# Kernel tuning notes

Hardware: AMD Instinct MI355X
Metric: run time of the kernel (lower is better)

The kernel has to match this reference:

```python
import jax, jax.numpy as jnp
import numpy as np

B, L, C = 8, 2048, 512
R, H, DK = 256, 8, 64
MASK_NEG = -2.0**15 + 1.0


def setup_inputs() -> dict:
    key = jax.random.key(0)
    ks = jax.random.split(key, 9)
    s = 1.0 / np.sqrt(C)
    return {
        "qx": jax.random.normal(ks[0], (B, L, C), jnp.float32),
        "kx": jax.random.normal(ks[1], (B, L, C), jnp.float32),
        "vx": jax.random.normal(ks[2], (B, L, C), jnp.float32),
        "addLoss": jnp.zeros((), jnp.float32),
        "maskPAD": jnp.ones((B, L, L), jnp.bool_),
        "Wp": jax.random.normal(ks[3], (R, C), jnp.float32) * s,
        "WQ": jax.random.normal(ks[4], (H * DK, C), jnp.float32) * s,
        "WK": jax.random.normal(ks[5], (H * DK, C), jnp.float32) * s,
        "WV": jax.random.normal(ks[6], (H * DK, C), jnp.float32) * s,
        "WO": jax.random.normal(ks[7], (C, H * DK), jnp.float32) * (1.0 / np.sqrt(H * DK)),
    }


def reference(qx, kx, vx, addLoss, maskPAD, Wp, WQ, WK, WV, WO):
    # linearLevel == 'l1', dropout treated as identity (eval), training losses included
    b, l, c = qx.shape
    r = Wp.shape[0]
    offI = (1.0 - jnp.eye(r, dtype=qx.dtype))  # ones_minus_I, [r, r]

    pScore = jnp.einsum('blc,rc->blr', vx, Wp)                       # [B, L, r]
    pad = (maskPAD[:, 0] == 0)                                       # [B, L]
    pScore = jnp.where(pad[:, :, None], MASK_NEG, pScore)
    pAlpha = jnp.swapaxes(jax.nn.softmax(pScore, axis=-2), -1, -2)   # [B, r, L]
    pAlpha_ = jax.nn.softmax(pScore, axis=-1)                        # [B, L, r]

    addLoss = addLoss + jnp.mean((jnp.einsum('brl,bsl->brs', pAlpha, pAlpha) * offI) ** 2)

    qr = pAlpha @ qx                                                 # [B, r, C]
    kr = pAlpha @ kx
    vr = pAlpha @ vx

    queries = (qr @ WQ.T).reshape(b, r, H, DK).transpose(0, 2, 1, 3)  # [B, H, r, dk]
    keys = (kr @ WK.T).reshape(b, r, H, DK).transpose(0, 2, 1, 3)
    values = (vr @ WV.T).reshape(b, r, H, DK).transpose(0, 2, 1, 3)

    scores = jnp.einsum('bhrd,bhsd->bhrs', queries, keys) / jnp.asarray(np.sqrt(DK), qx.dtype)
    alpha = jax.nn.softmax(scores, axis=-1)                          # [B, H, r, r]
    addLoss = addLoss + jnp.mean(alpha * offI)

    z = alpha @ values                                               # [B, H, r, dk]
    z = z.transpose(0, 2, 1, 3).reshape(b, r, H * DK)
    z = z @ WO.T                                                     # [B, r, C]

    addLoss = addLoss + jnp.mean((jnp.einsum('blr,bls->brs', pAlpha_, pAlpha_) * offI) ** 2)
    z = pAlpha_ @ z                                                  # [B, L, C]
    return z, scores, addLoss
```

## Files before the change

kernel.cpp:

```cpp
#include <hip/hip_runtime.h>

#define B_  8
#define L_  2048
#define C_  512
#define R_  256
#define H_  8
#define DK_ 64
#define HD_ 512
#define MASK_NEG (-32767.0f)

typedef __attribute__((ext_vector_type(8))) short short8;
typedef __attribute__((ext_vector_type(8))) unsigned short ushort8;
typedef __attribute__((ext_vector_type(4))) unsigned short ushort4_t;
typedef __attribute__((ext_vector_type(4))) float f32x4;
typedef unsigned short u16;

__device__ inline u16 bf16_rne(float x) {
    unsigned u = __float_as_uint(x);
    return (u16)((u + 0x7FFFu + ((u >> 16) & 1u)) >> 16);
}
__device__ inline unsigned cvt_hl(float x) {
    u16 hh = bf16_rne(x);
    float hf = __uint_as_float(((unsigned)hh) << 16);
    u16 ll = bf16_rne(x - hf);
    return (unsigned)hh | ((unsigned)ll << 16);
}

struct Ptr3 { const void* p0; const void* p1; const void* p2; };

__device__ inline float waveMax(float v) {
    #pragma unroll
    for (int o = 32; o; o >>= 1) v = fmaxf(v, __shfl_xor(v, o, 64));
    return v;
}
__device__ inline float waveSum(float v) {
    #pragma unroll
    for (int o = 32; o; o >>= 1) v += __shfl_xor(v, o, 64);
    return v;
}

#define GLL16(g, l) __builtin_amdgcn_global_load_lds( \
    (const __attribute__((address_space(1))) void*)(g), \
    (__attribute__((address_space(3))) void*)(l), 16, 0, 0)

template<int BN, int AMODE, int BMODE, int EPI, bool TRIPLE, int NTERM = 3, int KSPLIT = 1>
__global__ __launch_bounds__(256) void gemm_pl(
    Ptr3 aH, Ptr3 aL, Ptr3 bH, Ptr3 bL, Ptr3 cH, Ptr3 cL,
    Ptr3 cT1, Ptr3 cT2, int ldct, long long csT,
    int K, int lda, int ldb, int ldc, int divz,
    long long ash, long long bsh, long long csh,
    long long asb, long long bsb, long long csb,
    long long ksa, long long ksb, long long ksc,
    float scale)
{
    constexpr int NF = BN / 32;
    constexpr int XA = (NTERM == 3) ? 64 : 1;
    constexpr int XB = (NTERM == 3) ? BN : 1;
    __shared__ u16 Ahs[64][40], Als[XA][40];
    __shared__ u16 Bhs[BN][40], Bls[XB][40];

    const int gx = gridDim.x, gy = gridDim.y;
    const int nwg = gx * gy * gridDim.z;
    int flat = blockIdx.x + gx * (blockIdx.y + gy * blockIdx.z);
    {
        int q = nwg >> 3;
        int xcd = flat & 7, idx = flat >> 3;
        flat = xcd * q + idx;
    }
    const int bx = flat % gx;
    const int by = (flat / gx) % gy;
    const int z  = flat / (gx * gy);

    const int zb = z / divz;
    const int rem = z - zb * divz;
    const int zh = rem / KSPLIT, ks = rem - zh * KSPLIT;
    const int Keff = K / KSPLIT;
    const void* avH = TRIPLE ? (zb == 0 ? aH.p0 : zb == 1 ? aH.p1 : aH.p2) : aH.p0;
    const void* avL = TRIPLE ? (zb == 0 ? aL.p0 : zb == 1 ? aL.p1 : aL.p2) : aL.p0;
    const void* bvH = TRIPLE ? (zb == 0 ? bH.p0 : zb == 1 ? bH.p1 : bH.p2) : bH.p0;
    const void* bvL = TRIPLE ? (zb == 0 ? bL.p0 : zb == 1 ? bL.p1 : bL.p2) : bL.p0;
    void* cvH = (void*)(TRIPLE ? (zb == 0 ? cH.p0 : zb == 1 ? cH.p1 : cH.p2) : cH.p0);
    void* cvL = (void*)(TRIPLE ? (zb == 0 ? cL.p0 : zb == 1 ? cL.p1 : cL.p2) : cL.p0);
    void* cvT1 = (void*)(TRIPLE ? (zb == 0 ? cT1.p0 : zb == 1 ? cT1.p1 : cT1.p2) : cT1.p0);
    void* cvT2 = (void*)(TRIPLE ? (zb == 0 ? cT2.p0 : zb == 1 ? cT2.p1 : cT2.p2) : cT2.p0);
    const long long ao = (TRIPLE ? 0 : (long long)zb * asb) + (long long)zh * ash + (long long)ks * ksa;
    const long long bo = (TRIPLE ? 0 : (long long)zb * bsb) + (long long)zh * bsh + (long long)ks * ksb;
    const long long co = (TRIPLE ? 0 : (long long)zb * csb) + (long long)zh * csh + (long long)ks * ksc;
    const long long coT = (long long)zh * csT;

    const u16*   AHg = (const u16*)avH + ao;
    const u16*   ALg = (const u16*)avL + ao;
    const u16*   BHg = (const u16*)bvH + bo;
    const u16*   BLg = (const u16*)bvL + bo;
    const float* Bfg = (const float*)bvH + bo;
    float* Cf  = (float*)cvH + co;
    u16*   CHg = (u16*)cvH + co;
    u16*   CLg = (u16*)cvL + co;

    const int m0 = by * 64, n0 = bx * BN;
    const int tid = threadIdx.x;
    const int lane = tid & 63, w = tid >> 6;
    const int wrow = (w >> 1) * 32, wcol = (w & 1) * (BN / 2);
    const int l15 = lane & 15, lg = lane >> 4;

    f32x4 zero = {0.f, 0.f, 0.f, 0.f};
    f32x4 acc[2][NF];
    #pragma unroll
    for (int mf = 0; mf < 2; ++mf)
        #pragma unroll
        for (int nf = 0; nf < NF; ++nf) acc[mf][nf] = zero;

    for (int k0 = 0; k0 < Keff; k0 += 32) {
        {
            int row = tid >> 2, kc = (tid & 3) << 3;
            long long off = (long long)(m0 + row) * lda + (k0 + kc);
            *(ushort8*)&Ahs[row][kc] = *(const ushort8*)(AHg + off);
            if constexpr (NTERM == 3)
                *(ushort8*)&Als[row][kc] = *(const ushort8*)(ALg + off);
        }
        if (BMODE == 0) {
            #pragma unroll
            for (int t = tid; t < BN * 4; t += 256) {
                int row = t >> 2, kc = (t & 3) << 3;
                long long off = (long long)(n0 + row) * ldb + (k0 + kc);
                *(ushort8*)&Bhs[row][kc] = *(const ushort8*)(BHg + off);
                if constexpr (NTERM == 3)
                    *(ushort8*)&Bls[row][kc] = *(const ushort8*)(BLg + off);
            }
        } else {
            #pragma unroll
            for (int t = tid; t < BN * 4; t += 256) {
                int row = t >> 2, kc = (t & 3) << 3;
                const float* s = Bfg + (long long)(n0 + row) * ldb + (k0 + kc);
                float4 v0 = *(const float4*)s, v1 = *(const float4*)(s + 4);
                unsigned p0 = cvt_hl(v0.x), p1 = cvt_hl(v0.y), p2 = cvt_hl(v0.z), p3 = cvt_hl(v0.w);
                unsigned p4 = cvt_hl(v1.x), p5 = cvt_hl(v1.y), p6 = cvt_hl(v1.z), p7 = cvt_hl(v1.w);
                ushort8 h, l;
                h[0]=(u16)p0; h[1]=(u16)p1; h[2]=(u16)p2; h[3]=(u16)p3;
                h[4]=(u16)p4; h[5]=(u16)p5; h[6]=(u16)p6; h[7]=(u16)p7;
                l[0]=(u16)(p0>>16); l[1]=(u16)(p1>>16); l[2]=(u16)(p2>>16); l[3]=(u16)(p3>>16);
                l[4]=(u16)(p4>>16); l[5]=(u16)(p5>>16); l[6]=(u16)(p6>>16); l[7]=(u16)(p7>>16);
                *(ushort8*)&Bhs[row][kc] = h;
                if constexpr (NTERM == 3)
                    *(ushort8*)&Bls[row][kc] = l;
            }
        }
        __syncthreads();

        short8 a_h[2], a_l[2];
        a_h[0] = *(const short8*)&Ahs[wrow +      l15][lg * 8];
        a_h[1] = *(const short8*)&Ahs[wrow + 16 + l15][lg * 8];
        if constexpr (NTERM == 3) {
            a_l[0] = *(const short8*)&Als[wrow +      l15][lg * 8];
            a_l[1] = *(const short8*)&Als[wrow + 16 + l15][lg * 8];
        }
        #pragma unroll
        for (int nf = 0; nf < NF; ++nf) {
            short8 b_h = *(const short8*)&Bhs[wcol + nf * 16 + l15][lg * 8];
            if constexpr (NTERM == 3) {
                short8 b_l = *(const short8*)&Bls[wcol + nf * 16 + l15][lg * 8];
                #pragma unroll
                for (int mf = 0; mf < 2; ++mf) {
                    acc[mf][nf] = __builtin_amdgcn_mfma_f32_16x16x32_bf16(a_h[mf], b_h, acc[mf][nf], 0, 0, 0);
                    acc[mf][nf] = __builtin_amdgcn_mfma_f32_16x16x32_bf16(a_h[mf], b_l, acc[mf][nf], 0, 0, 0);
                    acc[mf][nf] = __builtin_amdgcn_mfma_f32_16x16x32_bf16(a_l[mf], b_h, acc[mf][nf], 0, 0, 0);
                }
            } else {
                #pragma unroll
                for (int mf = 0; mf < 2; ++mf)
                    acc[mf][nf] = __builtin_amdgcn_mfma_f32_16x16x32_bf16(a_h[mf], b_h, acc[mf][nf], 0, 0, 0);
            }
        }
        __syncthreads();
    }

    #pragma unroll
    for (int mf = 0; mf < 2; ++mf)
        #pragma unroll
        for (int nf = 0; nf < NF; ++nf) {
            int row = m0 + wrow + mf * 16 + lg * 4;
            int col = n0 + wcol + nf * 16 + l15;
            if constexpr (EPI == 0 || EPI == 3) {
                #pragma unroll
                for (int j = 0; j < 4; ++j)
                    Cf[(long long)(row + j) * ldc + col] = acc[mf][nf][j] * scale;
                if constexpr (EPI == 3) {
                    float* CfT = (float*)cvT1 + coT;
                    float4 v = make_float4(acc[mf][nf][0] * scale, acc[mf][nf][1] * scale,
                                           acc[mf][nf][2] * scale, acc[mf][nf][3] * scale);
                    *(float4*)(CfT + (long long)col * ldct + row) = v;
                }
            } else {
                unsigned p[4];
                #pragma unroll
                for (int j = 0; j < 4; ++j) {
                    p[j] = cvt_hl(acc[mf][nf][j] * scale);
                    if constexpr (EPI != 5) {
                        CHg[(long long)(row + j) * ldc + col] = (u16)p[j];
                        CLg[(long long)(row + j) * ldc + col] = (u16)(p[j] >> 16);
                    }
                }
                if constexpr (EPI == 4 || EPI == 5) {
                    u16* CTH = (u16*)cvT1 + coT;
                    u16* CTL = (u16*)cvT2 + coT;
                    ushort4_t h, l;
                    #pragma unroll
                    for (int j = 0; j < 4; ++j) { h[j] = (u16)p[j]; l[j] = (u16)(p[j] >> 16); }
                    *(ushort4_t*)(CTH + (long long)col * ldct + row) = h;
                    *(ushort4_t*)(CTL + (long long)col * ldct + row) = l;
                }
            }
        }
}

template<int EPI, bool TRIPLE, int NTERM, int KSPLIT, bool TRIANG = false>
__global__ __launch_bounds__(256) void gemm_gll(
    Ptr3 aH, Ptr3 aL, Ptr3 bH, Ptr3 bL, Ptr3 cH, Ptr3 cL,
    Ptr3 cT1, Ptr3 cT2, int ldct, long long csT,
    int K, int lda, int ldb, int ldc, int divz,
    long long ash, long long bsh, long long csh,
    long long ksa, long long ksb, long long ksc,
    float scale,
    const float* addLossIn = nullptr, const float* lossAcc = nullptr,
    const float* offArr = nullptr, float* lossOut = nullptr)
{
    constexpr int XA = (NTERM == 3) ? 128 : 1;
    __shared__ u16 Ahs[2][128][32];
    __shared__ u16 Bhs[2][128][32];
    __shared__ u16 Als[XA][32], Bls[XA][32];
    __shared__ float red2[4];

    const int gx = gridDim.x, gy = gridDim.y;
    const int nwg = gx * gy * gridDim.z;
    int flat = blockIdx.x + gx * (blockIdx.y + gy * blockIdx.z);
    {
        int q = nwg >> 3;
        int xcd = flat & 7, idx = flat >> 3;
        flat = xcd * q + idx;
    }
    const int bx = flat % gx;
    const int by = (flat / gx) % gy;
    const int z  = flat / (gx * gy);

    const int zb = z / divz;
    const int rem = z - zb * divz;
    const int zh = rem / KSPLIT, ks = rem - zh * KSPLIT;
    const int Keff = K / KSPLIT;
    const void* avH = TRIPLE ? (zb == 0 ? aH.p0 : zb == 1 ? aH.p1 : aH.p2) : aH.p0;
    const void* avL = TRIPLE ? (zb == 0 ? aL.p0 : zb == 1 ? aL.p1 : aL.p2) : aL.p0;
    const void* bvH = TRIPLE ? (zb == 0 ? bH.p0 : zb == 1 ? bH.p1 : bH.p2) : bH.p0;
    const void* bvL = TRIPLE ? (zb == 0 ? bL.p0 : zb == 1 ? bL.p1 : bL.p2) : bL.p0;
    void* cvH = (void*)(TRIPLE ? (zb == 0 ? cH.p0 : zb == 1 ? cH.p1 : cH.p2) : cH.p0);
    void* cvL = (void*)(TRIPLE ? (zb == 0 ? cL.p0 : zb == 1 ? cL.p1 : cL.p2) : cL.p0);
    void* cvT1 = (void*)(TRIPLE ? (zb == 0 ? cT1.p0 : zb == 1 ? cT1.p1 : cT1.p2) : cT1.p0);
    void* cvT2 = (void*)(TRIPLE ? (zb == 0 ? cT2.p0 : zb == 1 ? cT2.p1 : cT2.p2) : cT2.p0);
    const long long ao = (long long)zh * ash + (long long)ks * ksa;
    const long long bo = (long long)zh * bsh + (long long)ks * ksb;
    const long long co = (long long)zh * csh + (long long)ks * ksc;
    const long long coT = (long long)zh * csT;

    const u16* AHg = (const u16*)avH + ao;
    const u16* ALg = (const u16*)avL + ao;
    const u16* BHg = (const u16*)bvH + bo;
    const u16* BLg = (const u16*)bvL + bo;
    float* Cf  = (float*)cvH + co;
    u16*   CHg = (u16*)cvH + co;
    u16*   CLg = (u16*)cvL + co;

    int m0, n0;
    if constexpr (TRIANG) {
        m0 = (bx >= 1) ? 128 : 0;
        n0 = (bx == 2) ? 128 : 0;
    } else {
        m0 = by * 128; n0 = bx * 128;
    }
    const int tid = threadIdx.x;
    const int lane = tid & 63, w = tid >> 6;
    const int wrow = (w >> 1) * 64, wcol = (w & 1) * 64;
    const int l15 = lane & 15, lg = lane >> 4;

    f32x4 zero = {0.f, 0.f, 0.f, 0.f};
    f32x4 acc[4][4];
    #pragma unroll
    for (int mf = 0; mf < 4; ++mf)
        #pragma unroll
        for (int nf = 0; nf < 4; ++nf) acc[mf][nf] = zero;

    const int ric = lane >> 2;
    const int cc  = lane & 3;

    auto STAGE_HI = [&](int bufsel, int k0) {
        #pragma unroll
        for (int i = 0; i < 2; ++i) {
            int chunk = w * 2 + i;
            int row = chunk * 16 + ric;
            int gcol = ((cc ^ ((row >> 1) & 3)) << 3);
            GLL16(AHg + (long long)(m0 + row) * lda + (k0 + gcol), &Ahs[bufsel][chunk * 16][0]);
            GLL16(BHg + (long long)(n0 + row) * ldb + (k0 + gcol), &Bhs[bufsel][chunk * 16][0]);
        }
    };
    auto STAGE_LO = [&](int k0) {
        #pragma unroll
        for (int i = 0; i < 2; ++i) {
            int chunk = w * 2 + i;
            int row = chunk * 16 + ric;
            int gcol = ((cc ^ ((row >> 1) & 3)) << 3);
            GLL16(ALg + (long long)(m0 + row) * lda + (k0 + gcol), &Als[chunk * 16][0]);
            GLL16(BLg + (long long)(n0 + row) * ldb + (k0 + gcol), &Bls[chunk * 16][0]);
        }
    };

    const int nt = Keff / 32;
    int cur = 0;
    STAGE_HI(0, 0);

    for (int t = 0; t < nt; ++t) {
        if constexpr (NTERM == 3) STAGE_LO(t * 32);
        if (t + 1 < nt) {
            STAGE_HI(cur ^ 1, (t + 1) * 32);
            asm volatile("s_waitcnt vmcnt(4)" ::: "memory");
        } else {
            asm volatile("s_waitcnt vmcnt(0)" ::: "memory");
        }
        __builtin_amdgcn_s_barrier();

        short8 a_h[4], a_l[4];
        #pragma unroll
        for (int mf = 0; mf < 4; ++mf) {
            int ar = wrow + mf * 16 + l15;
            int ac = (lg ^ ((ar >> 1) & 3)) << 3;
            a_h[mf] = *(const short8*)&Ahs[cur][ar][ac];
            if constexpr (NTERM == 3) a_l[mf] = *(const short8*)&Als[ar][ac];
        }
        __builtin_amdgcn_s_setprio(1);
        #pragma unroll
        for (int nf = 0; nf < 4; ++nf) {
            int br = wcol + nf * 16 + l15;
            int bc = (lg ^ ((br >> 1) & 3)) << 3;
            short8 b_h = *(const short8*)&Bhs[cur][br][bc];
            if constexpr (NTERM == 3) {
                short8 b_l = *(const short8*)&Bls[br][bc];
                #pragma unroll
                for (int mf = 0; mf < 4; ++mf) {
                    acc[mf][nf] = __builtin_amdgcn_mfma_f32_16x16x32_bf16(a_h[mf], b_h, acc[mf][nf], 0, 0, 0);
                    acc[mf][nf] = __builtin_amdgcn_mfma_f32_16x16x32_bf16(a_h[mf], b_l, acc[mf][nf], 0, 0, 0);
                    acc[mf][nf] = __builtin_amdgcn_mfma_f32_16x16x32_bf16(a_l[mf], b_h, acc[mf][nf], 0, 0, 0);
                }
            } else {
                #pragma unroll
                for (int mf = 0; mf < 4; ++mf)
                    acc[mf][nf] = __builtin_amdgcn_mfma_f32_16x16x32_bf16(a_h[mf], b_h, acc[mf][nf], 0, 0, 0);
            }
        }
        __builtin_amdgcn_s_setprio(0);
        __builtin_amdgcn_s_barrier();
        cur ^= 1;
    }

    #pragma unroll
    for (int mf = 0; mf < 4; ++mf)
        #pragma unroll
        for (int nf = 0; nf < 4; ++nf) {
            int row = m0 + wrow + mf * 16 + lg * 4;
            int col = n0 + wcol + nf * 16 + l15;
            if constexpr (EPI == 0) {
                #pragma unroll
                for (int j = 0; j < 4; ++j)
                    Cf[(long long)(row + j) * ldc + col] = acc[mf][nf][j] * scale;
            } else {
                unsigned p[4];
                #pragma unroll
                for (int j = 0; j < 4; ++j) p[j] = cvt_hl(acc[mf][nf][j] * scale);
                if (cvH) {
                    #pragma unroll
                    for (int j = 0; j < 4; ++j) {
                        CHg[(long long)(row + j) * ldc + col] = (u16)p[j];
                        CLg[(long long)(row + j) * ldc + col] = (u16)(p[j] >> 16);
                    }
                }
                if constexpr (EPI == 3) {
                    if (cvT1) {
                        u16* CTH = (u16*)cvT1 + coT;
                        u16* CTL = (u16*)cvT2 + coT;
                        ushort4_t h, l;
                        #pragma unroll
                        for (int j = 0; j < 4; ++j) { h[j] = (u16)p[j]; l[j] = (u16)(p[j] >> 16); }
                        *(ushort4_t*)(CTH + (long long)col * ldct + row) = h;
                        *(ushort4_t*)(CTL + (long long)col * ldct + row) = l;
                    }
                }
            }
        }

    if (lossOut != nullptr && flat == 0) {
        float s = 0.0f;
        for (int i = tid; i < B_ * H_ * R_; i += 256) s += offArr[i];
        s = waveSum(s);
        if (lane == 0) red2[w] = s;
        __syncthreads();
        if (tid == 0) {
            float total = red2[0] + red2[1] + red2[2] + red2[3];
            lossOut[0] = addLossIn[0]
                       + lossAcc[0] * (1.0f / ((float)B_ * R_ * R_))
                       + total      * (1.0f / ((float)B_ * H_ * R_ * R_))
                       + lossAcc[2] * (1.0f / ((float)B_ * R_ * R_));
        }
    }
}

#define KS_ 4
#define NKS6_ 2
__global__ __launch_bounds__(256) void reduce_all(
    const float* __restrict__ G1, const float* __restrict__ G2,
    int nks, float* __restrict__ lossBase,
    const float* __restrict__ Cpart, Ptr3 dstH, Ptr3 dstL)
{
    __shared__ float red[4];
    int lane = threadIdx.x & 63, wid = threadIdx.x >> 6;
    if (blockIdx.x < 1024) {
        const long long N = (long long)B_ * R_ * R_;
        int seg = blockIdx.x >> 9;
        const float* G = seg ? G2 : G1;
        float* lossDst = lossBase + (seg ? 2 : 0);
        long long i4 = ((long long)(blockIdx.x & 511) * 256 + threadIdx.x) << 2;
        float s = 0.0f;
        if (i4 < N) {
            int e = (int)(i4 & (long long)(R_ * R_ - 1));
            int row = e >> 8, c0 = e & 255;
            if (!(row < 128 && c0 >= 128)) {
                float4 g = make_float4(0.f, 0.f, 0.f, 0.f);
                for (int ks = 0; ks < nks; ++ks) {
                    float4 v = *(const float4*)(G + (long long)ks * N + i4);
                    g.x += v.x; g.y += v.y; g.z += v.z; g.w += v.w;
                }
                float wgt = (row >= 128 && c0 < 128) ? 2.0f : 1.0f;
                if (row != c0 + 0) s += wgt * g.x * g.x;
                if (row != c0 + 1) s += wgt * g.y * g.y;
                if (row != c0 + 2) s += wgt * g.z * g.z;
                if (row != c0 + 3) s += wgt * g.w * g.w;
            }
        }
        #pragma unroll
        for (int o = 32; o; o >>= 1) s += __shfl_down(s, o, 64);
        if (lane == 0) red[wid] = s;
        __syncthreads();
        if (threadIdx.x == 0) atomicAdd(lossDst, red[0] + red[1] + red[2] + red[3]);
    } else {
        const long long T = (long long)B_ * R_ * C_;
        long long i4 = (long long)(blockIdx.x - 1024) * 256 + threadIdx.x;
        if (i4 >= 3 * (T >> 2)) return;
        int member = (int)(i4 / (T >> 2));
        long long rem = (i4 - (long long)member * (T >> 2)) << 2;
        float4 a = *(const float4*)(Cpart + (long long)member * T + rem);
        #pragma unroll
        for (int ks = 1; ks < NKS6_; ++ks) {
            float4 b = *(const float4*)(Cpart + (long long)ks * 3 * T + (long long)member * T + rem);
            a.x += b.x; a.y += b.y; a.z += b.z; a.w += b.w;
        }
        unsigned q0 = cvt_hl(a.x), q1 = cvt_hl(a.y), q2 = cvt_hl(a.z), q3 = cvt_hl(a.w);
        ushort4_t h, l;
        h[0]=(u16)q0; h[1]=(u16)q1; h[2]=(u16)q2; h[3]=(u16)q3;
        l[0]=(u16)(q0>>16); l[1]=(u16)(q1>>16); l[2]=(u16)(q2>>16); l[3]=(u16)(q3>>16);
        u16* dH = (u16*)(member == 0 ? dstH.p0 : member == 1 ? dstH.p1 : dstH.p2);
        u16* dL = (u16*)(member == 0 ? dstL.p0 : member == 1 ? dstL.p1 : dstL.p2);
        *(ushort4_t*)(dH + rem) = h;
        *(ushort4_t*)(dL + rem) = l;
    }
}

__global__ __launch_bounds__(256) void xpose_f32p3(
    Ptr3 src, Ptr3 dstH, Ptr3 dstL,
    int M, int N, long long ibs, long long obs, int divz)
{
    __shared__ float S[64][65];
    int z = blockIdx.z;
    int m = z / divz, b = z - m * divz;
    const float* ip = (const float*)(m == 0 ? src.p0 : m == 1 ? src.p1 : src.p2)
                      + (long long)b * ibs;
    u16* opH = (u16*)(m == 0 ? dstH.p0 : m == 1 ? dstH.p1 : dstH.p2) + (long long)b * obs;
    u16* opL = (u16*)(m == 0 ? dstL.p0 : m == 1 ? dstL.p1 : dstL.p2) + (long long)b * obs;
    int n0 = blockIdx.x * 64, m0 = blockIdx.y * 64;
    int t = threadIdx.x;
    int c4 = (t & 15) << 2, rq = t >> 4;
    #pragma unroll
    for (int p = 0; p < 4; ++p) {
        int r = p * 16 + rq;
        float4 v = *(const float4*)(ip + (long long)(m0 + r) * N + n0 + c4);
        S[r][c4+0]=v.x; S[r][c4+1]=v.y; S[r][c4+2]=v.z; S[r][c4+3]=v.w;
    }
    __syncthreads();
    #pragma unroll
    for (int p = 0; p < 4; ++p) {
        int nr = p * 16 + rq;
        unsigned q0 = cvt_hl(S[c4+0][nr]), q1 = cvt_hl(S[c4+1][nr]);
        unsigned q2 = cvt_hl(S[c4+2][nr]), q3 = cvt_hl(S[c4+3][nr]);
        ushort4_t h, l;
        h[0]=(u16)q0; h[1]=(u16)q1; h[2]=(u16)q2; h[3]=(u16)q3;
        l[0]=(u16)(q0>>16); l[1]=(u16)(q1>>16); l[2]=(u16)(q2>>16); l[3]=(u16)(q3>>16);
        long long ob = (long long)(n0 + nr) * M + m0 + c4;
        *(ushort4_t*)(opH + ob) = h;
        *(ushort4_t*)(opL + ob) = l;
    }
}

__global__ __launch_bounds__(256) void xpose_u16p(
    const u16* __restrict__ inH, const u16* __restrict__ inL,
    u16* __restrict__ outH, u16* __restrict__ outL,
    int M, int N, long long ibs, long long obs)
{
    __shared__ u16 SH[64][66], SL[64][66];
    const u16* ipH = inH + (long long)blockIdx.z * ibs;
    const u16* ipL = inL + (long long)blockIdx.z * ibs;
    u16* opH = outH + (long long)blockIdx.z * obs;
    u16* opL = outL + (long long)blockIdx.z * obs;
    int n0 = blockIdx.x * 64, m0 = blockIdx.y * 64;
    int t = threadIdx.x;
    int c4 = (t & 15) << 2, rq = t >> 4;
    #pragma unroll
    for (int p = 0; p < 4; ++p) {
        int r = p * 16 + rq;
        long long ib = (long long)(m0 + r) * N + n0 + c4;
        ushort4_t vh = *(const ushort4_t*)(ipH + ib);
        ushort4_t vl = *(const ushort4_t*)(ipL + ib);
        SH[r][c4+0]=vh[0]; SH[r][c4+1]=vh[1]; SH[r][c4+2]=vh[2]; SH[r][c4+3]=vh[3];
        SL[r][c4+0]=vl[0]; SL[r][c4+1]=vl[1]; SL[r][c4+2]=vl[2]; SL[r][c4+3]=vl[3];
    }
    __syncthreads();
    #pragma unroll
    for (int p = 0; p < 4; ++p) {
        int nr = p * 16 + rq;
        ushort4_t h, l;
        h[0]=SH[c4+0][nr]; h[1]=SH[c4+1][nr]; h[2]=SH[c4+2][nr]; h[3]=SH[c4+3][nr];
        l[0]=SL[c4+0][nr]; l[1]=SL[c4+1][nr]; l[2]=SL[c4+2][nr]; l[3]=SL[c4+3][nr];
        long long ob = (long long)(n0 + nr) * M + m0 + c4;
        *(ushort4_t*)(opH + ob) = h;
        *(ushort4_t*)(opL + ob) = l;
    }
}

__global__ __launch_bounds__(256) void conv_planes5(
    const float* __restrict__ s0, const float* __restrict__ s1, const float* __restrict__ s2,
    const float* __restrict__ s3, const float* __restrict__ s4,
    u16* h0, u16* l0, u16* h1, u16* l1, u16* h2, u16* l2,
    u16* h3, u16* l3, u16* h4, u16* l4,
    float* __restrict__ lossZero)
{
    if (blockIdx.x == 0 && threadIdx.x < 3) lossZero[threadIdx.x] = 0.0f;
    const int N0 = 32768, NW = 65536;
    int i = blockIdx.x * 256 + threadIdx.x;
    if (i >= N0 + 4 * NW) return;
    const float* s; u16* h; u16* l; int off;
    if (i < N0) { s = s0; h = h0; l = l0; off = i; }
    else {
        int j = i - N0, seg = j / NW;
        off = j - seg * NW;
        s = seg == 0 ? s1 : seg == 1 ? s2 : seg == 2 ? s3 : s4;
        h = seg == 0 ? h1 : seg == 1 ? h2 : seg == 2 ? h3 : h4;
        l = seg == 0 ? l1 : seg == 1 ? l2 : seg == 2 ? l3 : l4;
    }
    float4 v = ((const float4*)s)[off];
    unsigned p0 = cvt_hl(v.x), p1 = cvt_hl(v.y), p2 = cvt_hl(v.z), p3 = cvt_hl(v.w);
    ushort4_t hv, lv;
    hv[0]=(u16)p0; hv[1]=(u16)p1; hv[2]=(u16)p2; hv[3]=(u16)p3;
    lv[0]=(u16)(p0>>16); lv[1]=(u16)(p1>>16); lv[2]=(u16)(p2>>16); lv[3]=(u16)(p3>>16);
    ((ushort4_t*)h)[off] = hv;
    ((ushort4_t*)l)[off] = lv;
}

__global__ __launch_bounds__(256) void softmax_both(
    const float* __restrict__ pT, const float* __restrict__ pScore,
    const int* __restrict__ mask,
    u16* __restrict__ ltH, u16* __restrict__ ltL,
    u16* __restrict__ rH, u16* __restrict__ rL)
{
    __shared__ float sm[4], ss[4];
    int bxid = blockIdx.x;
    int lane = threadIdx.x & 63, wid = threadIdx.x >> 6;
    if (bxid < B_ * R_) {
        int zi = bxid;
        int b = zi >> 8;
        const float* row = pT + (long long)zi * L_;
        const int* mk = mask + (long long)b * L_ * L_;
        float vals[8];
        float mx = -3.4e38f;
        #pragma unroll
        for (int i = 0; i < 8; ++i) {
            int l = threadIdx.x + i * 256;
            float v = row[l];
            if (mk[l] == 0) v = MASK_NEG;
            vals[i] = v; mx = fmaxf(mx, v);
        }
        mx = waveMax(mx);
        if (lane == 0) sm[wid] = mx;
        __syncthreads();
        mx = fmaxf(fmaxf(sm[0], sm[1]), fmaxf(sm[2], sm[3]));
        float sum = 0.0f;
        #pragma unroll
        for (int i = 0; i < 8; ++i) { float e = __expf(vals[i] - mx); vals[i] = e; sum += e; }
        sum = waveSum(sum);
        if (lane == 0) ss[wid] = sum;
        __syncthreads();
        sum = ss[0] + ss[1] + ss[2] + ss[3];
        float inv = 1.0f / sum;
        long long base = (long long)zi * L_;
        #pragma unroll
        for (int i = 0; i < 8; ++i) {
            unsigned p = cvt_hl(vals[i] * inv);
            ltH[base + threadIdx.x + i * 256] = (u16)p;
            ltL[base + threadIdx.x + i * 256] = (u16)(p >> 16);
        }
    } else {
        long long z = (long long)(bxid - B_ * R_) * 4 + wid;
        int b = (int)(z >> 11), l = (int)(z & 2047);
        bool pad = (mask[(long long)b * L_ * L_ + l] == 0);
        float4 v = *(const float4*)(pScore + z * R_ + lane * 4);
        if (pad) { v.x = MASK_NEG; v.y = MASK_NEG; v.z = MASK_NEG; v.w = MASK_NEG; }
        float mx = waveMax(fmaxf(fmaxf(v.x, v.y), fmaxf(v.z, v.w)));
        float e0 = __expf(v.x - mx), e1 = __expf(v.y - mx);
        float e2 = __expf(v.z - mx), e3 = __expf(v.w - mx);
        float inv = 1.0f / waveSum(e0 + e1 + e2 + e3);
        unsigned p0 = cvt_hl(e0 * inv), p1 = cvt_hl(e1 * inv);
        unsigned p2 = cvt_hl(e2 * inv), p3 = cvt_hl(e3 * inv);
        ushort4_t h, lo;
        h[0]=(u16)p0; h[1]=(u16)p1; h[2]=(u16)p2; h[3]=(u16)p3;
        lo[0]=(u16)(p0>>16); lo[1]=(u16)(p1>>16); lo[2]=(u16)(p2>>16); lo[3]=(u16)(p3>>16);
        *(ushort4_t*)(rH + z * R_ + lane * 4) = h;
        *(ushort4_t*)(rL + z * R_ + lane * 4) = lo;
    }
}

__global__ __launch_bounds__(256) void softmax_alpha4(
    const float* __restrict__ scores, u16* __restrict__ aH, u16* __restrict__ aL,
    float* __restrict__ offArr)
{
    int lane = threadIdx.x & 63, wid = threadIdx.x >> 6;
    long long row = (long long)blockIdx.x * 4 + wid;
    int r = (int)(row & 255);
    float4 v = *(const float4*)(scores + row * 256 + lane * 4);
    float mx = waveMax(fmaxf(fmaxf(v.x, v.y), fmaxf(v.z, v.w)));
    float e0 = __expf(v.x - mx), e1 = __expf(v.y - mx);
    float e2 = __expf(v.z - mx), e3 = __expf(v.w - mx);
    float inv = 1.0f / waveSum(e0 + e1 + e2 + e3);
    float a0 = e0 * inv, a1 = e1 * inv, a2 = e2 * inv, a3 = e3 * inv;
    unsigned p0 = cvt_hl(a0), p1 = cvt_hl(a1), p2 = cvt_hl(a2), p3 = cvt_hl(a3);
    ushort4_t h, lo;
    h[0]=(u16)p0; h[1]=(u16)p1; h[2]=(u16)p2; h[3]=(u16)p3;
    lo[0]=(u16)(p0>>16); lo[1]=(u16)(p1>>16); lo[2]=(u16)(p2>>16); lo[3]=(u16)(p3>>16);
    *(ushort4_t*)(aH + row * 256 + lane * 4) = h;
    *(ushort4_t*)(aL + row * 256 + lane * 4) = lo;
    int c = lane * 4;
    float off = (c + 0 == r ? 0.0f : a0) + (c + 1 == r ? 0.0f : a1)
              + (c + 2 == r ? 0.0f : a2) + (c + 3 == r ? 0.0f : a3);
    off = waveSum(off);
    if (lane == 0) offArr[row] = off;
}

extern "C" void kernel_launch(void* const* d_in, const int* in_sizes, int n_in,
                              void* d_out, int out_size, void* d_ws, size_t ws_size,
                              hipStream_t stream)
{
    const float* qx = (const float*)d_in[0];
    const float* kx = (const float*)d_in[1];
    const float* vx = (const float*)d_in[2];
    const float* addLossIn = (const float*)d_in[3];
    const int* mask = (const int*)d_in[4];
    const float* Wp = (const float*)d_in[5];
    const float* WQ = (const float*)d_in[6];
    const float* WK = (const float*)d_in[7];
    const float* WV = (const float*)d_in[8];
    const float* WO = (const float*)d_in[9];

    float* zOut      = (float*)d_out;
    float* scoresOut = zOut + (long long)B_ * L_ * C_;
    float* lossOut   = scoresOut + (long long)B_ * H_ * R_ * R_;

    const long long S = (long long)B_ * L_ * R_;
    const long long T = (long long)B_ * R_ * C_;
    u16* cur = (u16*)d_ws;
    auto takeU = [&](long long n) { u16* p = cur; cur += n; return p; };
    auto takeF = [&](long long n) { float* p = (float*)cur; cur += 2 * n; return p; };

    float* pScore   = takeF(S);
    float* pScoreT  = takeF(S);
    u16* pAlphaH  = takeU(S);
    u16* pAlphaL  = takeU(S);
    u16* pAlpha_H = takeU(S);
    u16* pAlpha_L = takeU(S);
    u16* pATH     = takeU(S);
    u16* pATL     = takeU(S);
    u16* xTH0 = takeU(2*S); u16* xTL0 = takeU(2*S);
    u16* xTH1 = takeU(2*S); u16* xTL1 = takeU(2*S);
    u16* xTH2 = takeU(2*S); u16* xTL2 = takeU(2*S);
    const long long llRR = (long long)R_ * R_;
    float* Gpart  = takeF(2LL * KS_ * B_ * llRR);
    float* Cpart6 = takeF((long long)NKS6_ * 3 * T);
    u16* qrH = takeU(T); u16* qrL = takeU(T);
    u16* krH = takeU(T); u16* krL = takeU(T);
    u16* vrH = takeU(T); u16* vrL = takeU(T);
    u16* qpH = takeU(T); u16* qpL = takeU(T);
    u16* kpH = takeU(T); u16* kpL = takeU(T);
    u16* vpTH = takeU(T); u16* vpTL = takeU(T);
    u16* z1H = takeU(T); u16* z1L = takeU(T);
    u16* z2TH = takeU(T); u16* z2TL = takeU(T);
    u16* alphaH = takeU(S); u16* alphaL = takeU(S);
    u16* WpH = takeU((long long)R_ * C_); u16* WpL = takeU((long long)R_ * C_);
    u16* WQH = takeU((long long)HD_ * C_); u16* WQL = takeU((long long)HD_ * C_);
    u16* WKH = takeU((long long)HD_ * C_); u16* WKL = takeU((long long)HD_ * C_);
    u16* WVH = takeU((long long)HD_ * C_); u16* WVL = takeU((long long)HD_ * C_);
    u16* WOH = takeU((long long)HD_ * C_); u16* WOL = takeU((long long)HD_ * C_);
    float* loss   = takeF(16);
    float* offArr = takeF(B_ * H_ * R_);

    const Ptr3 N3{nullptr, nullptr, nullptr};
    auto P1 = [](const void* p) { return Ptr3{p, p, p}; };
    const long long llRL = (long long)R_ * L_, llLC = (long long)L_ * C_;
    const long long llRC = (long long)R_ * C_, llRHD = (long long)R_ * HD_;
    const long long llHRR = (long long)H_ * R_ * R_;
    const long long llCL = (long long)C_ * L_;
    float* Gpart2 = Gpart + (long long)KS_ * B_ * llRR;

    conv_planes5<<<1152, 256, 0, stream>>>(
        Wp, WQ, WK, WV, WO,
        WpH, WpL, WQH, WQL, WKH, WKL, WVH, WVL, WOH, WOL,
        loss);

    gemm_pl<64, 0, 2, 3, false><<<dim3(L_/64, R_/64, B_), 256, 0, stream>>>(
        P1(WpH), P1(WpL), P1(vx), N3, P1(pScoreT), N3,
        P1(pScore), N3, R_, llRL,
        C_, C_, C_, L_, B_,
        0, llLC, llRL, 0, 0, 0, 0, 0, 0, 1.0f);

    softmax_both<<<B_ * R_ + B_ * L_ / 4, 256, 0, stream>>>(
        pScoreT, pScore, mask, pAlphaH, pAlphaL, pAlpha_H, pAlpha_L);

    xpose_u16p<<<dim3(R_/64, L_/64, B_), 256, 0, stream>>>(
        pAlpha_H, pAlpha_L, pATH, pATL, L_, R_, llRL, llRL);

    gemm_gll<0, true, 1, KS_, true><<<dim3(3, 1, 2 * B_ * KS_), 256, 0, stream>>>(
        Ptr3{pAlphaH, pATH, pATH}, N3, Ptr3{pAlphaH, pATH, pATH}, N3,
        Ptr3{Gpart, Gpart2, Gpart2}, N3,
        N3, N3, 0, 0,
        L_, L_, L_, R_, B_ * KS_,
        llRL, llRL, llRR,
        L_ / KS_, L_ / KS_, (long long)B_ * llRR, 1.0f);

    xpose_f32p3<<<dim3(C_/64, L_/64, 3 * B_), 256, 0, stream>>>(
        Ptr3{qx, kx, vx}, Ptr3{xTH0, xTH1, xTH2}, Ptr3{xTL0, xTL1, xTL2},
        L_, C_, llLC, llCL, B_);

    gemm_gll<0, true, 3, NKS6_><<<dim3(C_/128, R_/128, 3 * B_ * NKS6_), 256, 0, stream>>>(
        P1(pAlphaH), P1(pAlphaL),
        Ptr3{xTH0, xTH1, xTH2}, Ptr3{xTL0, xTL1, xTL2},
        Ptr3{Cpart6, Cpart6 + T, Cpart6 + 2 * T}, N3,
        N3, N3, 0, 0,
        L_, L_, L_, C_, B_ * NKS6_,
        llRL, llCL, llRC,
        L_ / NKS6_, L_ / NKS6_, 3 * T, 1.0f);

    reduce_all<<<1024 + (int)(3 * (T >> 2) / 256), 256, 0, stream>>>(
        Gpart, Gpart2, KS_, loss,
        Cpart6, Ptr3{qrH, krH, vrH}, Ptr3{qrL, krL, vrL});

    gemm_gll<3, true, 3, 1><<<dim3(HD_/128, 2, 3 * B_), 256, 0, stream>>>(
        Ptr3{qrH, krH, vrH}, Ptr3{qrL, krL, vrL},
        Ptr3{WQH, WKH, WVH}, Ptr3{WQL, WKL, WVL},
        Ptr3{qpH, kpH, nullptr}, Ptr3{qpL, kpL, nullptr},
        Ptr3{nullptr, nullptr, vpTH}, Ptr3{nullptr, nullptr, vpTL}, R_, llRHD,
        C_, C_, C_, HD_, B_,
        llRC, 0, llRHD,
        0, 0, 0, 1.0f);

    gemm_pl<64, 0, 0, 0, false><<<dim3(4, 4, 64), 256, 0, stream>>>(
        P1(qpH), P1(qpL), P1(kpH), P1(kpL), P1(scoresOut), N3,
        N3, N3, 0, 0,
        DK_, HD_, HD_, R_, 8, 64, 64, llRR, llRHD, llRHD, llHRR,
        0, 0, 0, 0.125f);

    softmax_alpha4<<<B_ * H_ * R_ / 4, 256, 0, stream>>>(scoresOut, alphaH, alphaL, offArr);

    gemm_pl<64, 0, 0, 2, false><<<dim3(1, 4, 64), 256, 0, stream>>>(
        P1(alphaH), P1(alphaL), P1(vpTH), P1(vpTL), P1(z1H), P1(z1L),
        N3, N3, 0, 0,
        R_, R_, R_, HD_, 8, llRR, (long long)64 * R_, 64, llHRR, llRHD, llRHD,
        0, 0, 0, 1.0f);

    gemm_pl<64, 0, 0, 5, false><<<dim3(HD_/64, R_/64, B_), 256, 0, stream>>>(
        P1(z1H), P1(z1L), P1(WOH), P1(WOL), N3, N3,
        P1(z2TH), P1(z2TL), R_, llRC,
        HD_, HD_, HD_, C_, B_,
        llRHD, 0, llRC, 0, 0, 0, 0, 0, 0, 1.0f);

    gemm_gll<0, false, 3, 1><<<dim3(C_/128, L_/128, B_), 256, 0, stream>>>(
        P1(pAlpha_H), P1(pAlpha_L), P1(z2TH), P1(z2TL), P1(zOut), N3,
        N3, N3, 0, 0,
        R_, R_, R_, C_, B_,
        llRL, llRC, llLC,
        0, 0, 0, 1.0f,
        addLossIn, loss, offArr, lossOut);
}
```

Before: 281.8 us.

## Fuse attention softmax with alpha·V GEMM into one kernel

Replaces the separate softmax kernel and the alpha@V GEMM with a single kernel. Each block computes the softmax for 32 query rows, keeps the split bf16 hi/lo probabilities in shared memory, and multiplies them against V tiles with MFMA. This removes the global write and re-read of the alpha planes plus one launch. The cost is a smaller per-block tile with a simple, unpipelined V load loop, and 512 blocks in place of the earlier GEMM's tiling.

```diff
diff --git a/kernel.cpp b/kernel.cpp
--- a/kernel.cpp
+++ b/kernel.cpp
@@ -408,6 +408,93 @@
     }
 }
 
+__global__ __launch_bounds__(256) void softmax_pv(
+    const float* __restrict__ scores,
+    const u16* __restrict__ vpTH, const u16* __restrict__ vpTL,
+    u16* __restrict__ z1H, u16* __restrict__ z1L,
+    float* __restrict__ offArr)
+{
+    __shared__ u16 AH[32][264], AL[32][264];
+    __shared__ u16 BH[64][40], BL[64][40];
+    const int hd = blockIdx.x >> 3;
+    const int qt = blockIdx.x & 7;
+    const int q0 = qt * 32;
+    const int b  = hd >> 3, h = hd & 7;
+    const int tid = threadIdx.x;
+    const int lane = tid & 63, w = tid >> 6;
+    const int l15 = lane & 15, lg = lane >> 4;
+
+    const float* srow = scores + ((long long)hd * 256 + q0) * 256;
+    #pragma unroll
+    for (int i = 0; i < 8; ++i) {
+        int rr = w * 8 + i;
+        float4 v = *(const float4*)(srow + (long long)rr * 256 + lane * 4);
+        float mx = waveMax(fmaxf(fmaxf(v.x, v.y), fmaxf(v.z, v.w)));
+        float e0 = __expf(v.x - mx), e1 = __expf(v.y - mx);
+        float e2 = __expf(v.z - mx), e3 = __expf(v.w - mx);
+        float inv = 1.0f / waveSum(e0 + e1 + e2 + e3);
+        float a0 = e0 * inv, a1 = e1 * inv, a2 = e2 * inv, a3 = e3 * inv;
+        unsigned p0 = cvt_hl(a0), p1 = cvt_hl(a1), p2 = cvt_hl(a2), p3 = cvt_hl(a3);
+        ushort4_t hv, lv;
+        hv[0]=(u16)p0; hv[1]=(u16)p1; hv[2]=(u16)p2; hv[3]=(u16)p3;
+        lv[0]=(u16)(p0>>16); lv[1]=(u16)(p1>>16); lv[2]=(u16)(p2>>16); lv[3]=(u16)(p3>>16);
+        *(ushort4_t*)&AH[rr][lane * 4] = hv;
+        *(ushort4_t*)&AL[rr][lane * 4] = lv;
+        int rdiag = q0 + rr;
+        int c = lane * 4;
+        float off = (c + 0 == rdiag ? 0.0f : a0) + (c + 1 == rdiag ? 0.0f : a1)
+                  + (c + 2 == rdiag ? 0.0f : a2) + (c + 3 == rdiag ? 0.0f : a3);
+        off = waveSum(off);
+        if (lane == 0) offArr[(long long)hd * 256 + q0 + rr] = off;
+    }
+
+    const long long llRHD = (long long)R_ * HD_;
+    const u16* BHg = vpTH + (long long)b * llRHD + (long long)h * 64 * R_;
+    const u16* BLg = vpTL + (long long)b * llRHD + (long long)h * 64 * R_;
+    f32x4 zero = {0.f, 0.f, 0.f, 0.f};
+    f32x4 acc[2];
+    acc[0] = zero; acc[1] = zero;
+    for (int k0 = 0; k0 < 256; k0 += 32) {
+        {
+            int row = tid >> 2, kc = (tid & 3) << 3;
+            long long off = (long long)row * R_ + (k0 + kc);
+            *(ushort8*)&BH[row][kc] = *(const ushort8*)(BHg + off);
+            *(ushort8*)&BL[row][kc] = *(const ushort8*)(BLg + off);
+        }
+        __syncthreads();
+
+        short8 a_h[2], a_l[2];
+        #pragma unroll
+        for (int mf = 0; mf < 2; ++mf) {
+            a_h[mf] = *(const short8*)&AH[mf * 16 + l15][k0 + lg * 8];
+            a_l[mf] = *(const short8*)&AL[mf * 16 + l15][k0 + lg * 8];
+        }
+        short8 b_h = *(const short8*)&BH[w * 16 + l15][lg * 8];
+        short8 b_l = *(const short8*)&BL[w * 16 + l15][lg * 8];
+        #pragma unroll
+        for (int mf = 0; mf < 2; ++mf) {
+            acc[mf] = __builtin_amdgcn_mfma_f32_16x16x32_bf16(a_h[mf], b_h, acc[mf], 0, 0, 0);
+            acc[mf] = __builtin_amdgcn_mfma_f32_16x16x32_bf16(a_h[mf], b_l, acc[mf], 0, 0, 0);
+            acc[mf] = __builtin_amdgcn_mfma_f32_16x16x32_bf16(a_l[mf], b_h, acc[mf], 0, 0, 0);
+        }
+        __syncthreads();
+    }
+
+    u16* CH = z1H + (long long)b * llRHD + (long long)h * 64;
+    u16* CL = z1L + (long long)b * llRHD + (long long)h * 64;
+    #pragma unroll
+    for (int mf = 0; mf < 2; ++mf) {
+        int lrow = mf * 16 + lg * 4;
+        int lcol = w * 16 + l15;
+        #pragma unroll
+        for (int j = 0; j < 4; ++j) {
+            unsigned p = cvt_hl(acc[mf][j]);
+            CH[(long long)(q0 + lrow + j) * HD_ + lcol] = (u16)p;
+            CL[(long long)(q0 + lrow + j) * HD_ + lcol] = (u16)(p >> 16);
+        }
+    }
+}
+
 #define KS_ 4
 #define NKS6_ 2
 __global__ __launch_bounds__(256) void reduce_all(
@@ -629,32 +716,6 @@
     }
 }
 
-__global__ __launch_bounds__(256) void softmax_alpha4(
-    const float* __restrict__ scores, u16* __restrict__ aH, u16* __restrict__ aL,
-    float* __restrict__ offArr)
-{
-    int lane = threadIdx.x & 63, wid = threadIdx.x >> 6;
-    long long row = (long long)blockIdx.x * 4 + wid;
-    int r = (int)(row & 255);
-    float4 v = *(const float4*)(scores + row * 256 + lane * 4);
-    float mx = waveMax(fmaxf(fmaxf(v.x, v.y), fmaxf(v.z, v.w)));
-    float e0 = __expf(v.x - mx), e1 = __expf(v.y - mx);
-    float e2 = __expf(v.z - mx), e3 = __expf(v.w - mx);
-    float inv = 1.0f / waveSum(e0 + e1 + e2 + e3);
-    float a0 = e0 * inv, a1 = e1 * inv, a2 = e2 * inv, a3 = e3 * inv;
-    unsigned p0 = cvt_hl(a0), p1 = cvt_hl(a1), p2 = cvt_hl(a2), p3 = cvt_hl(a3);
-    ushort4_t h, lo;
-    h[0]=(u16)p0; h[1]=(u16)p1; h[2]=(u16)p2; h[3]=(u16)p3;
-    lo[0]=(u16)(p0>>16); lo[1]=(u16)(p1>>16); lo[2]=(u16)(p2>>16); lo[3]=(u16)(p3>>16);
-    *(ushort4_t*)(aH + row * 256 + lane * 4) = h;
-    *(ushort4_t*)(aL + row * 256 + lane * 4) = lo;
-    int c = lane * 4;
-    float off = (c + 0 == r ? 0.0f : a0) + (c + 1 == r ? 0.0f : a1)
-              + (c + 2 == r ? 0.0f : a2) + (c + 3 == r ? 0.0f : a3);
-    off = waveSum(off);
-    if (lane == 0) offArr[row] = off;
-}
-
 extern "C" void kernel_launch(void* const* d_in, const int* in_sizes, int n_in,
                               void* d_out, int out_size, void* d_ws, size_t ws_size,
                               hipStream_t stream)
@@ -702,7 +763,6 @@
     u16* vpTH = takeU(T); u16* vpTL = takeU(T);
     u16* z1H = takeU(T); u16* z1L = takeU(T);
     u16* z2TH = takeU(T); u16* z2TL = takeU(T);
-    u16* alphaH = takeU(S); u16* alphaL = takeU(S);
     u16* WpH = takeU((long long)R_ * C_); u16* WpL = takeU((long long)R_ * C_);
     u16* WQH = takeU((long long)HD_ * C_); u16* WQL = takeU((long long)HD_ * C_);
     u16* WKH = takeU((long long)HD_ * C_); u16* WKL = takeU((long long)HD_ * C_);
@@ -776,13 +836,8 @@
         DK_, HD_, HD_, R_, 8, 64, 64, llRR, llRHD, llRHD, llHRR,
         0, 0, 0, 0.125f);
 
-    softmax_alpha4<<<B_ * H_ * R_ / 4, 256, 0, stream>>>(scoresOut, alphaH, alphaL, offArr);
-
-    gemm_pl<64, 0, 0, 2, false><<<dim3(1, 4, 64), 256, 0, stream>>>(
-        P1(alphaH), P1(alphaL), P1(vpTH), P1(vpTL), P1(z1H), P1(z1L),
-        N3, N3, 0, 0,
-        R_, R_, R_, HD_, 8, llRR, (long long)64 * R_, 64, llHRR, llRHD, llRHD,
-        0, 0, 0, 1.0f);
+    softmax_pv<<<B_ * H_ * R_ / 32, 256, 0, stream>>>(
+        scoresOut, vpTH, vpTL, z1H, z1L, offArr);
 
     gemm_pl<64, 0, 0, 5, false><<<dim3(HD_/64, R_/64, B_), 256, 0, stream>>>(
         P1(z1H), P1(z1L), P1(WOH), P1(WOL), N3, N3,
```

Measured after the change: 280.7 us. About the same (-0.4%).
